# Kernel optimization log

Hardware: AMD Instinct MI355X
Metric: run time of the kernel (lower is better)

The kernel has to match this reference:

```python
import jax, jax.numpy as jnp
import numpy as np
from jax.scipy.special import xlogy

LAMBDA_XM = 0.05
LAMBDA_SEG2D = 1.0
BN_EPS = 1e-5


def setup_inputs() -> dict:
    key = jax.random.key(0)
    ks = jax.random.split(key, 40)
    S, N, Nv, B, Np, M, H, C, MID = 2, 240000, 80000, 2, 120000, 30000, 64, 20, 16
    Nimg = B * M
    f = lambda i, shape, s=0.05: jax.random.normal(ks[i], shape, jnp.float32) * s
    inp = {
        'img_feat': f(0, (S, Nimg, H), 1.0),
        'pts_feat': f(1, (S, Nv, H), 1.0),
        'coors_inv': jax.random.randint(ks[2], (S, N), 0, Nv),
        'labels': jax.random.randint(ks[3], (N,), 0, C),
        'img_label': jax.random.randint(ks[4], (Nimg,), 0, C),
        'p2img_idx': jax.random.randint(ks[5], (B, M), 0, Np),
        # multihead 3d classifiers (per scale): Linear(H,128)-ReLU-Linear(128,C)
        'w3a': f(6, (S, H, 128)), 'b3a': jnp.zeros((S, 128)),
        'w3b': f(7, (S, 128, C)), 'b3b': jnp.zeros((S, C)),
        # multihead fuse classifiers
        'wfa': f(8, (S, H, 128)), 'bfa': jnp.zeros((S, 128)),
        'wfb': f(9, (S, 128, C)), 'bfb': jnp.zeros((S, C)),
        # attention: fc1(H->H//4), fc2(H->H//4), fc3(H//2->2), conv1/conv2 (1x1 -> linear) + BN
        'fc1w': f(10, (S, H, MID)), 'fc1b': jnp.zeros((S, MID)),
        'fc2w': f(11, (S, H, MID)), 'fc2b': jnp.zeros((S, MID)),
        'fc3w': f(12, (S, 2 * MID, 2)), 'fc3b': jnp.zeros((S, 2)),
        'c1w': f(13, (S, H, H)), 'c1b': jnp.zeros((S, H)),
        'bn1g': jnp.ones((S, H)), 'bn1b': jnp.zeros((S, H)),
        'c2w': f(14, (S, H, H)), 'c2b': jnp.zeros((S, H)),
        'bn2g': jnp.ones((S, H)), 'bn2b': jnp.zeros((S, H)),
        # final classifier Linear(S*H,128)-ReLU-Linear(128,C)
        'clw1': f(15, (S * H, 128)), 'clb1': jnp.zeros((128,)),
        'clw2': f(16, (128, C)), 'clb2': jnp.zeros((C,)),
    }
    return inp


def _mlp2(x, w1, b1, w2, b2):
    return jax.nn.relu(x @ w1 + b1) @ w2 + b2


def _ce(logits, lab):
    logp = jax.nn.log_softmax(logits, -1)
    return -jnp.take_along_axis(logp, lab[:, None], axis=1).mean()


def _lovasz(probs, lab):
    # lovasz-softmax over all classes, averaged over present classes
    C = probs.shape[1]
    fg = jax.nn.one_hot(lab, C, dtype=probs.dtype)  # [N,C]
    errors = jnp.abs(fg - probs)

    def per_class(err_c, fg_c):
        order = jnp.argsort(-err_c)
        e = err_c[order]
        f = fg_c[order]
        gts = f.sum()
        inter = gts - jnp.cumsum(f)
        union = gts + jnp.cumsum(1.0 - f)
        jac = 1.0 - inter / union
        jac = jnp.concatenate([jac[:1], jac[1:] - jac[:-1]])
        return jnp.dot(e, jac)

    losses = jax.vmap(per_class)(errors.T, fg.T)  # [C]
    present = (fg.sum(0) > 0).astype(probs.dtype)
    return jnp.sum(losses * present) / jnp.maximum(present.sum(), 1.0)


def _seg_loss(logits, lab):
    return _ce(logits, lab) + _lovasz(jax.nn.softmax(logits, -1), lab)


def _convbn_relu(x, cw, cb, g, b):
    # 1x1 Conv1d == per-point linear; BN (training-mode batch stats over points)
    y = x @ cw + cb
    mu = y.mean(0)
    var = y.var(0)
    return jax.nn.relu((y - mu) * jax.lax.rsqrt(var + BN_EPS) * g + b)


def reference(img_feat, pts_feat, coors_inv, labels, img_label, p2img_idx,
              w3a, b3a, w3b, b3b, wfa, bfa, wfb, bfb,
              fc1w, fc1b, fc2w, fc2b, fc3w, fc3b,
              c1w, c1b, bn1g, bn1b, c2w, c2b, bn2g, bn2b,
              clw1, clb1, clw2, clb2):
    S, Nv, H = pts_feat.shape
    C = w3b.shape[-1]
    B, M = p2img_idx.shape
    N = labels.shape[0]
    Np = N // B
    # p2img_mapping: per-batch gather composed to one global gather (batch blocks are contiguous/equal)
    gidx = (jnp.arange(B)[:, None] * Np + p2img_idx).reshape(-1)  # [Nimg]

    loss = jnp.float32(0.0)
    feats = []
    for s in range(S):
        pred3d = _mlp2(pts_feat[s], w3a[s], b3a[s], w3b[s], b3b[s])  # [Nv,C]
        # voxelize_labels: majority vote per voxel (== unique+scatter_max count argmax)
        counts = jnp.zeros((Nv, C), jnp.float32).at[coors_inv[s], labels].add(1.0)
        vox_lab = jnp.argmax(counts, axis=1)  # [Nv]
        # gather voxel feats/preds to image-projected points (fused gather)
        idx = coors_inv[s][gidx]  # [Nimg]
        p = pts_feat[s][idx]      # [Nimg,H] pseudo feats
        pts_pred = pred3d[idx]    # [Nimg,C]
        v = img_feat[s]           # [Nimg,H] valid (image) feats
        # Attention fusion
        w = jax.nn.sigmoid(
            jnp.concatenate([p @ fc1w[s] + fc1b[s], v @ fc2w[s] + fc2b[s]], -1) @ fc3w[s] + fc3b[s])  # [Nimg,2]
        fuse = (_convbn_relu(p, c1w[s], c1b[s], bn1g[s], bn1b[s]) * w[:, 0:1]
                + _convbn_relu(v, c2w[s], c2b[s], bn2g[s], bn2b[s]) * w[:, 1:2])
        feats.append(fuse)
        fuse_pred = _mlp2(fuse, wfa[s], bfa[s], wfb[s], bfb[s])
        loss = loss + _seg_loss(pred3d, vox_lab)
        loss = loss + _seg_loss(fuse_pred, img_label) * LAMBDA_SEG2D / S
        # F.kl_div(log_softmax(pts_pred), softmax(fuse_pred)), reduction='mean' over all elements
        pf = jax.nn.softmax(fuse_pred, -1)
        kl = jnp.mean(xlogy(pf, pf) - pf * jax.nn.log_softmax(pts_pred, -1))
        loss = loss + kl * LAMBDA_XM / S
    img_logits = _mlp2(jnp.concatenate(feats, -1), clw1, clb1, clw2, clb2)
    loss = loss + _seg_loss(img_logits, img_label)
    return loss
```

## Files before the change

kernel.cpp:

```cpp
#include <hip/hip_runtime.h>
#include <stdint.h>

static constexpr int NV   = 80000;
static constexpr int NPT  = 240000;
static constexpr int NIMG = 60000;
static constexpr int Hh   = 64;
static constexpr int Cc   = 20;
static constexpr int NPp  = 120000;
static constexpr int Mm   = 30000;
static constexpr int NB     = 8192;
static constexpr int NCH    = 16;
static constexpr int NBLK_GA  = (NIMG + 63) / 64;
static constexpr int NBLK_MLP = NV / 64;
static constexpr int NBLK_CNT = (NPT + 255) / 256;
static constexpr int NBLK_FILL_NV = (NV + 255) / 256;
static constexpr int NBLK_FILL_NI = (NIMG + 255) / 256;
static constexpr int NBLK_HIST = Cc * NCH;
static constexpr int NBLK_IDX  = (NIMG + 255) / 256;
#define BN_EPS 1e-5f

using bf16x8 = __attribute__((ext_vector_type(8))) short;
using f32x4  = __attribute__((ext_vector_type(4))) float;

__device__ __forceinline__ float waveReduce(float v) {
  #pragma unroll
  for (int o = 32; o > 0; o >>= 1) v += __shfl_down(v, o);
  return v;
}
__device__ __forceinline__ short f2bf(float f) {
  uint32_t u = __float_as_uint(f);
  return (short)((u + 0x7FFFu + ((u >> 16) & 1u)) >> 16);
}
__device__ __forceinline__ float bf2f(uint32_t h) { return __uint_as_float(h << 16); }
__device__ __forceinline__ uint32_t pk2(float a, float b) {
  return ((uint32_t)(uint16_t)f2bf(a)) | ((uint32_t)(uint16_t)f2bf(b) << 16);
}

struct PackDesc { const float* src; short* dst; int K, Nr, nt; };
struct PackArgs { PackDesc d[14]; };

__global__ void __launch_bounds__(256)
k_pack_zero(PackArgs pa,
            const float* __restrict__ fc1w, const float* __restrict__ fc1b,
            const float* __restrict__ fc2w, const float* __restrict__ fc2b,
            const float* __restrict__ fc3w, const float* __restrict__ fc3b,
            float* __restrict__ attEffs,
            uint4* __restrict__ zb, int zq,
            const int* __restrict__ ci0, const int* __restrict__ ci1,
            const int* __restrict__ p2img,
// ... 28 lines not shown
      int k = kt * 32 + (lane >> 4) * 8 + j;
      int n = nt * 16 + (lane & 15);
      float v = (n < Nr) ? src[(size_t)k * Nr + n] : 0.f;
      dst[idx] = f2bf(v);
    }
  }
  if (bid < 2 && threadIdx.x < 64) {
    int s = bid, t = threadIdx.x;
    const float* f1w = fc1w + s * 64 * 16; const float* f1b = fc1b + s * 16;
    const float* f2w = fc2w + s * 64 * 16; const float* f2b = fc2b + s * 16;
    const float* f3w = fc3w + s * 64;      const float* f3b = fc3b + s * 2;
    float* aE = attEffs + s * 320;
    float p0 = 0.f, p1 = 0.f, v0 = 0.f, v1 = 0.f;
    #pragma unroll
    for (int j = 0; j < 16; j++) {
      p0 = fmaf(f1w[t * 16 + j], f3w[j * 2], p0);
      p1 = fmaf(f1w[t * 16 + j], f3w[j * 2 + 1], p1);
      v0 = fmaf(f2w[t * 16 + j], f3w[(16 + j) * 2], v0);
      v1 = fmaf(f2w[t * 16 + j], f3w[(16 + j) * 2 + 1], v1);
    }
    aE[t * 2] = p0; aE[t * 2 + 1] = p1;
    aE[128 + t * 2] = v0; aE[128 + t * 2 + 1] = v1;
    if (t == 0) {
      float b0 = f3b[0], b1 = f3b[1];
      for (int j = 0; j < 16; j++) {
        b0 += f1b[j] * f3w[j * 2] + f2b[j] * f3w[(16 + j) * 2];
        b1 += f1b[j] * f3w[j * 2 + 1] + f2b[j] * f3w[(16 + j) * 2 + 1];
      }
      aE[256] = b0; aE[257] = b1;
    }
  }
}

__device__ void scanbin_body(const uint32_t* __restrict__ Hb, const uint32_t* __restrict__ HFb,
                             int n, int call, float* __restrict__ lossesC5,
                             int* __restrict__ gts5, int cls) {
  __shared__ int sWC[4], sWF[4];
  __shared__ float sRedF[4];
  int t = threadIdx.x;
  int lane = t & 63, w = t >> 6;
  const uint32_t* Hc  = Hb  + (size_t)cls * NB;
  const uint32_t* HFc = HFb + (size_t)cls * NB;
  int locC = 0, locF = 0;
  #pragma unroll
  for (int i = 0; i < 8; i++) {
    uint4 cv = *(const uint4*)(Hc  + t * 32 + i * 4);
    uint4 fv = *(const uint4*)(HFc + t * 32 + i * 4);
    locC += (int)(cv.x + cv.y + cv.z + cv.w);
    locF += (int)(fv.x + fv.y + fv.z + fv.w);
  }
  int sc = locC, sf = locF;
  #pragma unroll
  for (int o = 1; o < 64; o <<= 1) {
    int a = __shfl_up(sc, o);
    int b = __shfl_up(sf, o);
    if (lane >= o) { sc += a; sf += b; }
  }
  if (lane == 63) { sWC[w] = sc; sWF[w] = sf; }
  __syncthreads();
  int offC = 0, offF = 0, Ftot = 0;
  #pragma unroll
  for (int ww = 0; ww < 4; ww++) {
    int fc = sWF[ww];
    Ftot += fc;
    if (ww < w) { offC += sWC[ww]; offF += fc; }
  }
  int runC = offC + sc - locC;
  int runF = offF + sf - locF;
  float gts = (float)Ftot;
  float contrib = 0.f;
  #pragma unroll
  for (int i = 0; i < 8; i++) {
    uint4 cv = *(const uint4*)(Hc  + t * 32 + i * 4);
    uint4 fv = *(const uint4*)(HFc + t * 32 + i * 4);
    uint32_t ca[4] = {cv.x, cv.y, cv.z, cv.w};
    uint32_t fa[4] = {fv.x, fv.y, fv.z, fv.w};
    #pragma unroll
    for (int j = 0; j < 4; j++) {
      int cnt = (int)ca[j], fgc = (int)fa[j];
      runC += cnt; runF += fgc;
      if (cnt > 0 && Ftot > 0) {
        float r0 = (float)(n - runC);
        float F0 = (float)(Ftot - runF);
        float r1 = r0 + (float)cnt;
        float F1 = F0 + (float)fgc;
        float emean = __uint_as_float((uint32_t)(t * 32 + i * 4 + j) << 17);
        contrib += emean * (r1 / (gts + r1 - F1) - r0 / (gts + r0 - F0));
      }
    }
  }
  contrib = waveReduce(contrib);
  if (lane == 0) sRedF[w] = contrib;
  __syncthreads();
  if (t == 0) {
    lossesC5[call * 32 + cls] = (Ftot > 0) ? (sRedF[0] + sRedF[1] + sRedF[2] + sRedF[3]) : 0.f;
    gts5[call * 32 + cls] = Ftot;
  }
}

template<int D>
__device__ __forceinline__ void mfma_mlp_body(const short* sXb, short* sH,
    int r0, int rows,
    const short* __restrict__ pw1, const float* __restrict__ B1,
    const short* __restrict__ pw2, const float* __restrict__ B2,
    float* __restrict__ Out) {
  constexpr int LDB = D + 8;
  constexpr int KT1 = D / 32;
  const int t = threadIdx.x;
  const int lane = t & 63, w = t >> 6;
  const int m = lane & 15, quad = lane >> 4;
  const int rowA = 16 * w + m;
  bf16x8 a1[KT1];
  #pragma unroll
  for (int kt = 0; kt < KT1; kt++)
    a1[kt] = *(const bf16x8*)(sXb + rowA * LDB + kt * 32 + quad * 8);
  const bf16x8* b1 = (const bf16x8*)pw1;
  #pragma unroll
  for (int nt = 0; nt < 8; nt++) {
    f32x4 c = {0.f, 0.f, 0.f, 0.f};
    #pragma unroll
    for (int kt = 0; kt < KT1; kt++)
      c = __builtin_amdgcn_mfma_f32_16x16x32_bf16(a1[kt], b1[(kt * 8 + nt) * 64 + lane], c, 0, 0, 0);
    int col = nt * 16 + m;
    float bc = B1[col];
    #pragma unroll
    for (int reg = 0; reg < 4; reg++)
      sH[(16 * w + quad * 4 + reg) * 136 + col] = f2bf(fmaxf(c[reg] + bc, 0.f));
  }
  __syncthreads();
  bf16x8 a2[4];
  #pragma unroll
  for (int kt = 0; kt < 4; kt++)
    a2[kt] = *(const bf16x8*)(sH + rowA * 136 + kt * 32 + quad * 8);
  const bf16x8* b2 = (const bf16x8*)pw2;
  #pragma unroll
  for (int nt = 0; nt < 2; nt++) {
    f32x4 c = {0.f, 0.f, 0.f, 0.f};
    #pragma unroll
    for (int kt = 0; kt < 4; kt++)
      c = __builtin_amdgcn_mfma_f32_16x16x32_bf16(a2[kt], b2[(kt * 2 + nt) * 64 + lane], c, 0, 0, 0);
    int col = nt * 16 + m;
    if (col < Cc) {
      float bc = B2[col];
      #pragma unroll
      for (int reg = 0; reg < 4; reg++) {
        int gr = r0 + 16 * w + quad * 4 + reg;
        if (gr < rows) Out[(size_t)gr * Cc + col] = c[reg] + bc;
      }
    }
  }
}

__device__ void mlp64_body(int bid0, const float* __restrict__ X,
    const short* __restrict__ pw1, const float* __restrict__ B1,
    const short* __restrict__ pw2, const float* __restrict__ B2,
    float* __restrict__ Out, int rows, char* smem) {
  short* sXb = (short*)smem;
  short* sH  = (short*)(smem + 9216);
  int t = threadIdx.x, r0 = bid0 * 64;
  for (int i = t; i < 1024; i += 256) {
    int r = i >> 4, k4 = (i & 15) * 4;
    int gr = r0 + r;
    float4 v = (gr < rows) ? *(const float4*)(X + (size_t)gr * 64 + k4)
                           : make_float4(0.f, 0.f, 0.f, 0.f);
    uint2 p; p.x = pk2(v.x, v.y); p.y = pk2(v.z, v.w);
    *(uint2*)(sXb + r * 72 + k4) = p;
  }
  __syncthreads();
  mfma_mlp_body<64>(sXb, sH, r0, rows, pw1, B1, pw2, B2, Out);
}

__device__ void mlp128_body(int bid0, const uint16_t* __restrict__ Xh,
    const short* __restrict__ pw1, const float* __restrict__ B1,
    const short* __restrict__ pw2, const float* __restrict__ B2,
    float* __restrict__ Out, char* smem) {
  short* sXb = (short*)smem;
  short* sH  = (short*)(smem + 17408);
  int t = threadIdx.x, r0 = bid0 * 64;
  for (int i = t; i < 2048; i += 256) {
    int r = i >> 5, k4 = (i & 31) * 4;
    int gr = r0 + r;
    uint2 p = (gr < NIMG) ? *(const uint2*)(Xh + (size_t)gr * 128 + k4) : make_uint2(0u, 0u);
    *(uint2*)(sXb + r * 136 + k4) = p;
  }
  __syncthreads();
  mfma_mlp_body<128>(sXb, sH, r0, NIMG, pw1, B1, pw2, B2, Out);
}

__device__ void cnt_body(int bid0, const int* __restrict__ ci, const int* __restrict__ labels,
                         int* __restrict__ counts) {
  int i = bid0 * 256 + threadIdx.x;
  if (i < NPT) atomicAdd(&counts[(size_t)ci[i] * Cc + labels[i]], 1);
}

__device__ void colred_body(int bid0, const float* __restrict__ partials,
                            float* __restrict__ red64) {
  int t = threadIdx.x, j = bid0;
  float v = 0.f;
  for (int b = j; b < NBLK_GA; b += 64) v += partials[(size_t)b * 256 + t];
  red64[j * 256 + t] = v;
}

__device__ void fill_body(int bid0, const float* __restrict__ logits,
                          const int* __restrict__ lab, const int* __restrict__ vcnt,
                          int n, uint16_t* __restrict__ E,
                          float ceScale, float* __restrict__ lossAcc,
                          const float* __restrict__ pred3d, const int* __restrict__ idxg,
                          float klScale) {
  int i = bid0 * 256 + threadIdx.x;
  float total = 0.f;
  if (i < n) {
    int lb;
    if (vcnt) {
      const int* crow = vcnt + (size_t)i * Cc;
      int best = crow[0], arg = 0;
      #pragma unroll
      for (int k = 1; k < Cc; k++) {
        int ck = crow[k];
        if (ck > best) { best = ck; arg = k; }
      }
      lb = arg;
    } else {
      lb = lab[i];
    }
    const float* l = logits + (size_t)i * Cc;
    float m = l[0];
    #pragma unroll
    for (int c = 1; c < Cc; c++) m = fmaxf(m, l[c]);
    float ex[Cc]; float se = 0.f;
    #pragma unroll
    for (int c = 0; c < Cc; c++) { ex[c] = expf(l[c] - m); se += ex[c]; }
    float inv = 1.f / se;
    float lse = logf(se);
    total = -(l[lb] - m - lse) * ceScale;
    #pragma unroll
    for (int c = 0; c < Cc; c++) {
      float prob = ex[c] * inv;
      int fg = (c == lb) ? 1 : 0;
      float err = fg ? (1.f - prob) : prob;
      err = fmaxf(err, 0.f);
      uint32_t key = __float_as_uint(err) >> 17;
      E[(size_t)c * n + i] = (uint16_t)((key << 1) | (uint32_t)fg);
    }
    if (pred3d) {
      const float* q = pred3d + (size_t)idxg[i] * Cc;
      float mq = q[0];
      #pragma unroll
      for (int c = 1; c < Cc; c++) mq = fmaxf(mq, q[c]);
      float sq = 0.f;
      #pragma unroll
      for (int c = 0; c < Cc; c++) sq += expf(q[c] - mq);
      float lsq = logf(sq);
      float kl = 0.f;
      #pragma unroll
      for (int c = 0; c < Cc; c++) {
        float lf = l[c] - m - lse;
        float pf = ex[c] * inv;
        float lq = q[c] - mq - lsq;
        kl += pf * (lf - lq);
      }
      total += kl * klScale;
    }
  }
  total = waveReduce(total);
  __shared__ float sh[4];
  int lane = threadIdx.x & 63, w = threadIdx.x >> 6;
  if (lane == 0) sh[w] = total;
  __syncthreads();
  if (threadIdx.x == 0) atomicAdd(lossAcc, sh[0] + sh[1] + sh[2] + sh[3]);
}

__device__ void hist_body(int bid0, const uint16_t* __restrict__ E, int n,
                          uint32_t* __restrict__ H, uint32_t* __restrict__ HF, char* smem) {
  uint32_t* lcf = (uint32_t*)smem;
  int t = threadIdx.x;
  int cls = bid0 / NCH, ch = bid0 - cls * NCH;
  int CHsz = (n + NCH - 1) / NCH;
  int i0 = ch * CHsz;
  int i1 = min(n, i0 + CHsz);
  for (int b = t; b < NB; b += 256) lcf[b] = 0u;
  __syncthreads();
  const uint16_t* Ec = E + (size_t)cls * n;
  for (int i = i0 + t; i < i1; i += 256) {
    uint32_t p = Ec[i];
    atomicAdd(&lcf[p >> 1], 0x10000u | (p & 1u));
  }
  __syncthreads();
  uint32_t* Hc  = H  + (size_t)cls * NB;
  uint32_t* HFc = HF + (size_t)cls * NB;
  for (int b = t; b < NB; b += 256) {
    uint32_t v = lcf[b];
    if (v) {
      atomicAdd(&Hc[b], v >> 16);
      uint32_t f = v & 0xFFFFu;
      if (f) atomicAdd(&HFc[b], f);
    }
  }
}

__device__ void gatt_body(int bid0, const float* __restrict__ pts, const int* __restrict__ idx,
                          const float* __restrict__ img,
                          const short* __restrict__ pc1, const float* __restrict__ c1b,
                          const short* __restrict__ pc2, const float* __restrict__ c2b,
                          const float* __restrict__ attEff,
                          uint16_t* __restrict__ y1, uint16_t* __restrict__ y2,
                          float* __restrict__ attw, float* __restrict__ partials,
                          char* smem) {
  short* sP = (short*)smem;
  short* sV = (short*)(smem + 9216);
  float* sAtt  = (float*)(smem + 18432);
  float* sStat = (float*)(smem + 20480);
  int t = threadIdx.x;
  int r0 = bid0 * 64;
  for (int i = t; i < 1024; i += 256) {
    int r = i >> 4, q = i & 15;
    int gr = r0 + r;
    float4 vp = make_float4(0.f, 0.f, 0.f, 0.f), vv = vp;
    if (gr < NIMG) {
      vp = *(const float4*)(pts + (size_t)idx[gr] * 64 + q * 4);
      vv = *(const float4*)(img + (size_t)gr * 64 + q * 4);
    }
    uint2 pp, qv;
    pp.x = pk2(vp.x, vp.y); pp.y = pk2(vp.z, vp.w);
    qv.x = pk2(vv.x, vv.y); qv.y = pk2(vv.z, vv.w);
    *(uint2*)(sP + r * 72 + q * 4) = pp;
    *(uint2*)(sV + r * 72 + q * 4) = qv;
  }
  __syncthreads();
  {
// ... 64 lines not shown
      base[32] = s2;
      base[48] = q2;
    }
  }
  __syncthreads();
  {
    int kind = t >> 6, col = t & 63;
    int nt = col >> 4, mm = col & 15;
    float v = 0.f;
    #pragma unroll
    for (int ww = 0; ww < 4; ww++)
      v += sStat[(ww * 4 + nt) * 64 + kind * 16 + mm];
    partials[(size_t)bid0 * 256 + kind * 64 + col] = v;
  }
  if (t < 64) {
    int gr = r0 + t;
    if (gr < NIMG) {
      float l0 = attEff[256] + sAtt[t * 8] + sAtt[t * 8 + 2] + sAtt[t * 8 + 4] + sAtt[t * 8 + 6];
      float l1 = attEff[257] + sAtt[t * 8 + 1] + sAtt[t * 8 + 3] + sAtt[t * 8 + 5] + sAtt[t * 8 + 7];
      attw[gr * 2]     = 1.f / (1.f + expf(-l0));
      attw[gr * 2 + 1] = 1.f / (1.f + expf(-l1));
    }
  }
}

__device__ void fusemlp_body(int bid0,
    const uint16_t* __restrict__ y1, const uint16_t* __restrict__ y2,
    const float* __restrict__ attw, const float* __restrict__ red64,
    const float* __restrict__ g1, const float* __restrict__ be1,
    const float* __restrict__ g2, const float* __restrict__ be2,
    uint16_t* __restrict__ feats, int s64,
    const short* __restrict__ pw1, const float* __restrict__ B1,
    const short* __restrict__ pw2, const float* __restrict__ B2,
    float* __restrict__ Out, char* smem) {
  short* sXb = (short*)smem;
  short* sH  = (short*)(smem + 9216);
  float* sBn = (float*)(smem + 9216 + 17408);
  int t = threadIdx.x, r0 = bid0 * 64;
  float acc = 0.f;
  #pragma unroll 8
  for (int b = 0; b < 64; b++) acc += red64[b * 256 + t];
  float* sSum = (float*)sH;
  sSum[t] = acc;
  __syncthreads();
  if (t < 64) {
    float nn = (float)NIMG;
    float mu1 = sSum[t] / nn;
    float var1 = sSum[64 + t] / nn - mu1 * mu1;
    float a1 = g1[t] / sqrtf(var1 + BN_EPS);
    sBn[t] = a1; sBn[64 + t] = be1[t] - mu1 * a1;
    float mu2 = sSum[128 + t] / nn;
    float var2 = sSum[192 + t] / nn - mu2 * mu2;
    float a2 = g2[t] / sqrtf(var2 + BN_EPS);
    sBn[128 + t] = a2; sBn[192 + t] = be2[t] - mu2 * a2;
  }
  __syncthreads();
  for (int i = t; i < 1024; i += 256) {
    int r = i >> 4, q = i & 15;
    int gr = r0 + r;
    uint2 zp = make_uint2(0u, 0u);
    if (gr < NIMG) {
      float4 a1 = *(const float4*)(sBn + q * 4);
      float4 c1 = *(const float4*)(sBn + 64 + q * 4);
      float4 a2 = *(const float4*)(sBn + 128 + q * 4);
      float4 c2 = *(const float4*)(sBn + 192 + q * 4);
      uint2 u1 = *(const uint2*)(y1 + (size_t)gr * 64 + q * 4);
      uint2 u2 = *(const uint2*)(y2 + (size_t)gr * 64 + q * 4);
      float w0 = attw[gr * 2], w1 = attw[gr * 2 + 1];
      float zx = fmaxf(fmaf(bf2f(u1.x & 0xffff), a1.x, c1.x), 0.f) * w0
               + fmaxf(fmaf(bf2f(u2.x & 0xffff), a2.x, c2.x), 0.f) * w1;
      float zy = fmaxf(fmaf(bf2f(u1.x >> 16),   a1.y, c1.y), 0.f) * w0
               + fmaxf(fmaf(bf2f(u2.x >> 16),   a2.y, c2.y), 0.f) * w1;
      float zz = fmaxf(fmaf(bf2f(u1.y & 0xffff), a1.z, c1.z), 0.f) * w0
               + fmaxf(fmaf(bf2f(u2.y & 0xffff), a2.z, c2.z), 0.f) * w1;
      float zw = fmaxf(fmaf(bf2f(u1.y >> 16),   a1.w, c1.w), 0.f) * w0
               + fmaxf(fmaf(bf2f(u2.y >> 16),   a2.w, c2.w), 0.f) * w1;
      zp.x = pk2(zx, zy); zp.y = pk2(zz, zw);
      *(uint2*)(feats + (size_t)gr * 128 + s64 + q * 4) = zp;
    }
    *(uint2*)(sXb + r * 72 + q * 4) = zp;
  }
  __syncthreads();
  mfma_mlp_body<64>(sXb, sH, r0, NIMG, pw1, B1, pw2, B2, Out);
}

__global__ void __launch_bounds__(256)
k_mega2(const float* __restrict__ pf0, const float* __restrict__ pf1,
        const int* __restrict__ idx0, const int* __restrict__ idx1,
        const float* __restrict__ if0, const float* __restrict__ if1,
        const short* pc1w0, const short* pc1w1, const short* pc2w0, const short* pc2w1,
        const float* c1b, const float* c2b, const float* attEffs,
        uint16_t* y1a, uint16_t* y2a, uint16_t* y1b, uint16_t* y2b,
        float* attw0, float* attw1, float* partials0, float* partials1,
        const short* pw3a0, const float* b3a, const short* pw3b0, const float* b3b,
        const short* pw3a1, const short* pw3b1,
        float* pred3d0, float* pred3d1,
        const int* __restrict__ ci0, const int* __restrict__ ci1,
        const int* __restrict__ labels,
        int* __restrict__ counts0, int* __restrict__ counts1) {
  __shared__ char smem[26624];
  int bid = blockIdx.x;
  if (bid < NBLK_GA) {
    gatt_body(bid, pf0, idx0, if0, pc1w0, c1b, pc2w0, c2b, attEffs,
              y1a, y2a, attw0, partials0, smem);
    return;
  }
  bid -= NBLK_GA;
  if (bid < NBLK_GA) {
    gatt_body(bid, pf1, idx1, if1, pc1w1, c1b + 64, pc2w1, c2b + 64, attEffs + 320,
              y1b, y2b, attw1, partials1, smem);
    return;
  }
  bid -= NBLK_GA;
  if (bid < NBLK_MLP) { mlp64_body(bid, pf0, pw3a0, b3a, pw3b0, b3b, pred3d0, NV, smem); return; }
  bid -= NBLK_MLP;
  if (bid < NBLK_MLP) { mlp64_body(bid, pf1, pw3a1, b3a + 128, pw3b1, b3b + Cc, pred3d1, NV, smem); return; }
  bid -= NBLK_MLP;
  if (bid < NBLK_CNT) { cnt_body(bid, ci0, labels, counts0); return; }
  cnt_body(bid - NBLK_CNT, ci1, labels, counts1);
}

__global__ void __launch_bounds__(256)
k_fill_colred(const float* __restrict__ l0, const int* __restrict__ vc0, uint16_t* __restrict__ E0,
              const float* __restrict__ l1, const int* __restrict__ vc1, uint16_t* __restrict__ E1,
              float ce, float* __restrict__ lossAcc,
              const float* partials0, float* red64_0,
              const float* partials1, float* red64_1) {
  int bid = blockIdx.x;
  if (bid < NBLK_FILL_NV) {
    fill_body(bid, l0, nullptr, vc0, NV, E0, ce, lossAcc, nullptr, nullptr, 0.f);
    return;
  }
  bid -= NBLK_FILL_NV;
  if (bid < NBLK_FILL_NV) {
    fill_body(bid, l1, nullptr, vc1, NV, E1, ce, lossAcc, nullptr, nullptr, 0.f);
    return;
  }
  bid -= NBLK_FILL_NV;
  if (bid < 64) { colred_body(bid, partials0, red64_0); return; }
  colred_body(bid - 64, partials1, red64_1);
}

__global__ void __launch_bounds__(256)
k_fuse2_hist2(const uint16_t* y1a, const uint16_t* y2a, const float* attw0, const float* red64_0,
              const uint16_t* y1b, const uint16_t* y2b, const float* attw1, const float* red64_1,
              const float* bn1g, const float* bn1b, const float* bn2g, const float* bn2b,
              uint16_t* feats,
              const short* pwfa0, const float* bfa, const short* pwfb0, const float* bfb,
              const short* pwfa1, const short* pwfb1,
              float* fusepred0, float* fusepred1,
              const uint16_t* __restrict__ E0, uint32_t* H0, uint32_t* HF0,
              const uint16_t* __restrict__ E1, uint32_t* H2, uint32_t* HF2) {
  __shared__ char smem[32768];
  int bid = blockIdx.x;
  if (bid < NBLK_GA) {
    fusemlp_body(bid, y1a, y2a, attw0, red64_0, bn1g, bn1b, bn2g, bn2b, feats, 0,
                 pwfa0, bfa, pwfb0, bfb, fusepred0, smem);
    return;
  }
  bid -= NBLK_GA;
  if (bid < NBLK_GA) {
    fusemlp_body(bid, y1b, y2b, attw1, red64_1, bn1g + 64, bn1b + 64, bn2g + 64, bn2b + 64,
                 feats, 64, pwfa1, bfa + 128, pwfb1, bfb + Cc, fusepred1, smem);
    return;
  }
  bid -= NBLK_GA;
  if (bid < NBLK_HIST) { hist_body(bid, E0, NV, H0, HF0, smem); return; }
  hist_body(bid - NBLK_HIST, E1, NV, H2, HF2, smem);
}

__global__ void __launch_bounds__(256)
k_finx2(const uint16_t* __restrict__ feats,
        const short* pcl1, const float* clb1, const short* pcl2, const float* clb2,
        float* finalpred,
        const float* fusepred0, const float* pred3d0, const int* idx0, uint16_t* E0w,
        const float* fusepred1, const float* pred3d1, const int* idx1, uint16_t* E1w,
        const int* __restrict__ img_label, float ce, float kl, float* lossAcc,
        const uint32_t* H0, const uint32_t* HF0,
        const uint32_t* H2, const uint32_t* HF2,
        float* lossesC5, int* gts5) {
  __shared__ char smem[34816];
  int bid = blockIdx.x;
  if (bid < NBLK_GA) { mlp128_body(bid, feats, pcl1, clb1, pcl2, clb2, finalpred, smem); return; }
  bid -= NBLK_GA;
  if (bid < NBLK_FILL_NI) {
    fill_body(bid, fusepred0, img_label, nullptr, NIMG, E0w, ce, lossAcc, pred3d0, idx0, kl);
    return;
  }
  bid -= NBLK_FILL_NI;
  if (bid < NBLK_FILL_NI) {
    fill_body(bid, fusepred1, img_label, nullptr, NIMG, E1w, ce, lossAcc, pred3d1, idx1, kl);
    return;
  }
  bid -= NBLK_FILL_NI;
  if (bid < Cc) { scanbin_body(H0, HF0, NV, 0, lossesC5, gts5, bid); return; }
  scanbin_body(H2, HF2, NV, 2, lossesC5, gts5, bid - Cc);
}

__global__ void __launch_bounds__(256)
k_hist2_fill(const uint16_t* __restrict__ E0, uint32_t* H1, uint32_t* HF1,
             const uint16_t* __restrict__ E1, uint32_t* H3, uint32_t* HF3,
             const float* __restrict__ finalpred, const int* __restrict__ img_label,
             uint16_t* __restrict__ E2, float ce, float* lossAcc) {
  __shared__ char smem[32768];
  int bid = blockIdx.x;
  if (bid < NBLK_HIST) { hist_body(bid, E0, NIMG, H1, HF1, smem); return; }
  bid -= NBLK_HIST;
  if (bid < NBLK_HIST) { hist_body(bid, E1, NIMG, H3, HF3, smem); return; }
  fill_body(bid - NBLK_HIST, finalpred, img_label, nullptr, NIMG, E2, ce, lossAcc,
            nullptr, nullptr, 0.f);
}

__global__ void __launch_bounds__(256)
k_hist_scan2(const uint16_t* __restrict__ E2, uint32_t* H4, uint32_t* HF4,
             const uint32_t* H1, const uint32_t* HF1,
             const uint32_t* H3, const uint32_t* HF3,
             float* lossesC5, int* gts5) {
  __shared__ char smem[32768];
  int bid = blockIdx.x;
  if (bid < NBLK_HIST) { hist_body(bid, E2, NIMG, H4, HF4, smem); return; }
  bid -= NBLK_HIST;
  if (bid < Cc) { scanbin_body(H1, HF1, NIMG, 1, lossesC5, gts5, bid); return; }
  scanbin_body(H3, HF3, NIMG, 3, lossesC5, gts5, bid - Cc);
}

__global__ void __launch_bounds__(256)
k_scanbin5(const uint32_t* Hb, const uint32_t* HFb, int n, int call,
           float* lossesC5, int* gts5) {
  scanbin_body(Hb, HFb, n, call, lossesC5, gts5, blockIdx.x);
}

__global__ void k_final(const float* __restrict__ lossAcc,
                        const float* __restrict__ lossesC5, const int* __restrict__ gts5,
                        float* __restrict__ out) {
  const float coefs[5] = {1.0f, 0.5f, 1.0f, 0.5f, 1.0f};
  float loss = lossAcc[0];
  for (int call = 0; call < 5; call++) {
    float s = 0.f; int np = 0;
    for (int c = 0; c < Cc; c++)
      if (gts5[call * 32 + c] > 0) { s += lossesC5[call * 32 + c]; np++; }
    loss += coefs[call] * s / (float)(np > 0 ? np : 1);
  }
  out[0] = loss;
}

extern "C" void kernel_launch(void* const* d_in, const int* in_sizes, int n_in,
                              void* d_out, int out_size, void* d_ws, size_t ws_size,
                              hipStream_t stream) {
  const float* img_feat = (const float*)d_in[0];
  const float* pts_feat = (const float*)d_in[1];
  const int* coors_inv  = (const int*)d_in[2];
  const int* labels     = (const int*)d_in[3];
  const int* img_label  = (const int*)d_in[4];
  const int* p2img      = (const int*)d_in[5];
  const float* w3a = (const float*)d_in[6];
  const float* b3a = (const float*)d_in[7];
  const float* w3b = (const float*)d_in[8];
  const float* b3b = (const float*)d_in[9];
  const float* wfa = (const float*)d_in[10];
  const float* bfa = (const float*)d_in[11];
  const float* wfb = (const float*)d_in[12];
  const float* bfb = (const float*)d_in[13];
// ... 2 lines not shown
  const float* fc2w = (const float*)d_in[16];
  const float* fc2b = (const float*)d_in[17];
  const float* fc3w = (const float*)d_in[18];
  const float* fc3b = (const float*)d_in[19];
  const float* c1w  = (const float*)d_in[20];
  const float* c1b  = (const float*)d_in[21];
  const float* bn1g = (const float*)d_in[22];
  const float* bn1b = (const float*)d_in[23];
  const float* c2w  = (const float*)d_in[24];
  const float* c2b  = (const float*)d_in[25];
  const float* bn2g = (const float*)d_in[26];
  const float* bn2b = (const float*)d_in[27];
  const float* clw1 = (const float*)d_in[28];
  const float* clb1 = (const float*)d_in[29];
  const float* clw2 = (const float*)d_in[30];
  const float* clb2 = (const float*)d_in[31];
  (void)in_sizes; (void)n_in; (void)out_size; (void)ws_size;

  char* ws = (char*)d_ws;
  size_t off = 0;
  auto alloc = [&](size_t bytes) { void* p = ws + off; off += (bytes + 255) & ~(size_t)255; return p; };
  uint16_t* feats = (uint16_t*)alloc((size_t)NIMG * 128 * 2);
  float* pred3d0 = (float*)alloc((size_t)NV * Cc * 4);
  float* pred3d1 = (float*)alloc((size_t)NV * Cc * 4);
  int* idx0 = (int*)alloc((size_t)NIMG * 4);
  int* idx1 = (int*)alloc((size_t)NIMG * 4);
  uint16_t* y1a = (uint16_t*)alloc((size_t)NIMG * Hh * 2);
  uint16_t* y2a = (uint16_t*)alloc((size_t)NIMG * Hh * 2);
  uint16_t* y1b = (uint16_t*)alloc((size_t)NIMG * Hh * 2);
  uint16_t* y2b = (uint16_t*)alloc((size_t)NIMG * Hh * 2);
  uint16_t* E0 = (uint16_t*)alloc((size_t)Cc * NV * 2);
  uint16_t* E1 = (uint16_t*)alloc((size_t)Cc * NV * 2);
  uint16_t* E2 = (uint16_t*)alloc((size_t)Cc * NIMG * 2);
  float* partials0 = (float*)alloc((size_t)NBLK_GA * 256 * 4);
  float* partials1 = (float*)alloc((size_t)NBLK_GA * 256 * 4);
  float* red64_0 = (float*)alloc(64 * 256 * 4);
  float* red64_1 = (float*)alloc(64 * 256 * 4);
  float* attw0 = (float*)alloc((size_t)NIMG * 2 * 4);
  float* attw1 = (float*)alloc((size_t)NIMG * 2 * 4);
  float* fusepred0 = (float*)alloc((size_t)NIMG * Cc * 4);
  float* fusepred1 = (float*)alloc((size_t)NIMG * Cc * 4);
  float* finalpred = (float*)alloc((size_t)NIMG * Cc * 4);
  short* pwAll = (short*)alloc(86016 * 2);
  short* pw3a0 = pwAll,          * pw3a1 = pwAll + 8192;
  short* pwfa0 = pwAll + 16384,  * pwfa1 = pwAll + 24576;
  short* pw3b0 = pwAll + 32768,  * pw3b1 = pwAll + 36864;
  short* pwfb0 = pwAll + 40960,  * pwfb1 = pwAll + 45056;
  short* pcl1  = pwAll + 49152;
  short* pcl2  = pwAll + 65536;
  short* pc1w0 = pwAll + 69632,  * pc1w1 = pwAll + 73728;
  short* pc2w0 = pwAll + 77824,  * pc2w1 = pwAll + 81920;
  float* attEffs = (float*)alloc(2 * 320 * 4);
  size_t zsize = 1024 + (size_t)5 * 2 * Cc * NB * 4 + (size_t)2 * NV * Cc * 4;
  char* zbase = (char*)alloc(zsize);
  float* lossAcc  = (float*)zbase;
  float* lossesC5 = (float*)zbase + 32;
  int*   gts5     = (int*)((float*)zbase + 192);
  uint32_t* Hbase = (uint32_t*)(zbase + 1024);
  auto Hc  = [&](int call) { return Hbase + (size_t)call * 2 * Cc * NB; };
  auto HFc = [&](int call) { return Hbase + (size_t)call * 2 * Cc * NB + (size_t)Cc * NB; };
  int* counts0 = (int*)(zbase + 1024 + (size_t)5 * 2 * Cc * NB * 4);
  int* counts1 = counts0 + (size_t)NV * Cc;
  int zq = (int)(zsize / 16);

  const float kl = 0.025f / ((float)NIMG * Cc);
  const float* pf0 = pts_feat;
  const float* pf1 = pts_feat + (size_t)NV * Hh;
  const float* if0 = img_feat;
  const float* if1 = img_feat + (size_t)NIMG * Hh;
  const int* ci0 = coors_inv;
  const int* ci1 = coors_inv + NPT;

  PackArgs pa;
  pa.d[0]  = {w3a,        pw3a0, 64, 128, 8};
  pa.d[1]  = {w3a + 8192, pw3a1, 64, 128, 8};
  pa.d[2]  = {wfa,        pwfa0, 64, 128, 8};
  pa.d[3]  = {wfa + 8192, pwfa1, 64, 128, 8};
  pa.d[4]  = {w3b,        pw3b0, 128, 20, 2};
  pa.d[5]  = {w3b + 2560, pw3b1, 128, 20, 2};
  pa.d[6]  = {wfb,        pwfb0, 128, 20, 2};
  pa.d[7]  = {wfb + 2560, pwfb1, 128, 20, 2};
  pa.d[8]  = {clw1,       pcl1, 128, 128, 8};
  pa.d[9]  = {clw2,       pcl2, 128, 20, 2};
  pa.d[10] = {c1w,        pc1w0, 64, 64, 4};
  pa.d[11] = {c1w + 4096, pc1w1, 64, 64, 4};
  pa.d[12] = {c2w,        pc2w0, 64, 64, 4};
  pa.d[13] = {c2w + 4096, pc2w1, 64, 64, 4};
  k_pack_zero<<<384 + 2 * NBLK_IDX, 256, 0, stream>>>(
      pa, fc1w, fc1b, fc2w, fc2b, fc3w, fc3b, attEffs,
      (uint4*)zbase, zq, ci0, ci1, p2img, idx0, idx1);

  k_mega2<<<2 * NBLK_GA + 2 * NBLK_MLP + 2 * NBLK_CNT, 256, 0, stream>>>(
      pf0, pf1, idx0, idx1, if0, if1,
      pc1w0, pc1w1, pc2w0, pc2w1, c1b, c2b, attEffs,
      y1a, y2a, y1b, y2b, attw0, attw1, partials0, partials1,
      pw3a0, b3a, pw3b0, b3b, pw3a1, pw3b1, pred3d0, pred3d1,
      ci0, ci1, labels, counts0, counts1);

  k_fill_colred<<<2 * NBLK_FILL_NV + 128, 256, 0, stream>>>(
      pred3d0, counts0, E0, pred3d1, counts1, E1, 1.0f / NV, lossAcc,
      partials0, red64_0, partials1, red64_1);

  k_fuse2_hist2<<<2 * NBLK_GA + 2 * NBLK_HIST, 256, 0, stream>>>(
      y1a, y2a, attw0, red64_0, y1b, y2b, attw1, red64_1,
      bn1g, bn1b, bn2g, bn2b, feats,
      pwfa0, bfa, pwfb0, bfb, pwfa1, pwfb1, fusepred0, fusepred1,
      E0, Hc(0), HFc(0), E1, Hc(2), HFc(2));

  k_finx2<<<NBLK_GA + 2 * NBLK_FILL_NI + 2 * Cc, 256, 0, stream>>>(
      feats, pcl1, clb1, pcl2, clb2, finalpred,
      fusepred0, pred3d0, idx0, E0,
      fusepred1, pred3d1, idx1, E1,
      img_label, 0.5f / NIMG, kl, lossAcc,
      Hc(0), HFc(0), Hc(2), HFc(2), lossesC5, gts5);

  k_hist2_fill<<<2 * NBLK_HIST + NBLK_FILL_NI, 256, 0, stream>>>(
      E0, Hc(1), HFc(1), E1, Hc(3), HFc(3),
      finalpred, img_label, E2, 1.0f / NIMG, lossAcc);

  k_hist_scan2<<<NBLK_HIST + 2 * Cc, 256, 0, stream>>>(
      E2, Hc(4), HFc(4), Hc(1), HFc(1), Hc(3), HFc(3), lossesC5, gts5);

  k_scanbin5<<<Cc, 256, 0, stream>>>(Hc(4), HFc(4), NIMG, 4, lossesC5, gts5);

  k_final<<<1, 1, 0, stream>>>(lossAcc, lossesC5, gts5, (float*)d_out);
}
```

Measured before the change: 347.1 us.

## Fuse loss/error computation into MLP epilogues and pack histogram bins into 64-bit

The fuse-MLP and final-classifier kernels now keep their logits in LDS and compute CE, KL and Lovasz error keys directly in a tile epilogue. This removes the fusepred/finalpred global buffers and the separate fill passes, which drops one kernel launch and reshuffles the histogram work into earlier kernels. Count and foreground histograms are merged into one interleaved 64-bit array, so each bin takes a single 64-bit atomic and scans do one vector load per pair. The cost is that only 64 of 256 threads per block run the epilogue loss, and separate E3/E4 buffers are added.

```diff
diff --git a/kernel.cpp b/kernel.cpp
--- a/kernel.cpp
+++ b/kernel.cpp
@@ -14,7 +14,6 @@
 static constexpr int NBLK_MLP = NV / 64;
 static constexpr int NBLK_CNT = (NPT + 255) / 256;
 static constexpr int NBLK_FILL_NV = (NV + 255) / 256;
-static constexpr int NBLK_FILL_NI = (NIMG + 255) / 256;
 static constexpr int NBLK_HIST = Cc * NCH;
 static constexpr int NBLK_IDX  = (NIMG + 255) / 256;
 #define BN_EPS 1e-5f
@@ -109,22 +108,20 @@
   }
 }
 
-__device__ void scanbin_body(const uint32_t* __restrict__ Hb, const uint32_t* __restrict__ HFb,
+__device__ void scanbin_body(const unsigned long long* __restrict__ H64,
                              int n, int call, float* __restrict__ lossesC5,
                              int* __restrict__ gts5, int cls) {
   __shared__ int sWC[4], sWF[4];
   __shared__ float sRedF[4];
   int t = threadIdx.x;
   int lane = t & 63, w = t >> 6;
-  const uint32_t* Hc  = Hb  + (size_t)cls * NB;
-  const uint32_t* HFc = HFb + (size_t)cls * NB;
+  const uint4* Hv = (const uint4*)(H64 + (size_t)cls * NB + (size_t)t * 32);
   int locC = 0, locF = 0;
   #pragma unroll
-  for (int i = 0; i < 8; i++) {
-    uint4 cv = *(const uint4*)(Hc  + t * 32 + i * 4);
-    uint4 fv = *(const uint4*)(HFc + t * 32 + i * 4);
-    locC += (int)(cv.x + cv.y + cv.z + cv.w);
-    locF += (int)(fv.x + fv.y + fv.z + fv.w);
+  for (int i = 0; i < 16; i++) {
+    uint4 u = Hv[i];
+    locF += (int)(u.x + u.z);
+    locC += (int)(u.y + u.w);
   }
   int sc = locC, sf = locF;
   #pragma unroll
@@ -147,21 +144,18 @@
   float gts = (float)Ftot;
   float contrib = 0.f;
   #pragma unroll
-  for (int i = 0; i < 8; i++) {
-    uint4 cv = *(const uint4*)(Hc  + t * 32 + i * 4);
-    uint4 fv = *(const uint4*)(HFc + t * 32 + i * 4);
-    uint32_t ca[4] = {cv.x, cv.y, cv.z, cv.w};
-    uint32_t fa[4] = {fv.x, fv.y, fv.z, fv.w};
-    #pragma unroll
-    for (int j = 0; j < 4; j++) {
-      int cnt = (int)ca[j], fgc = (int)fa[j];
+  for (int i = 0; i < 16; i++) {
+    uint4 u = Hv[i];
+    #pragma unroll
+    for (int j = 0; j < 2; j++) {
+      int cnt = (int)(j ? u.w : u.y), fgc = (int)(j ? u.z : u.x);
       runC += cnt; runF += fgc;
       if (cnt > 0 && Ftot > 0) {
         float r0 = (float)(n - runC);
         float F0 = (float)(Ftot - runF);
         float r1 = r0 + (float)cnt;
         float F1 = F0 + (float)fgc;
-        float emean = __uint_as_float((uint32_t)(t * 32 + i * 4 + j) << 17);
+        float emean = __uint_as_float((uint32_t)(t * 32 + i * 2 + j) << 17);
         contrib += emean * (r1 / (gts + r1 - F1) - r0 / (gts + r0 - F0));
       }
     }
@@ -175,8 +169,63 @@
   }
 }
 
-template<int D>
-__device__ __forceinline__ void mfma_mlp_body(const short* sXb, short* sH,
+__device__ void tile_loss(const float* __restrict__ sL, int r0, int rows, int n,
+                          const int* __restrict__ lab, uint16_t* __restrict__ E,
+                          float ceScale, float* __restrict__ lossAcc,
+                          const float* __restrict__ pred3d, const int* __restrict__ idxg,
+                          float klScale) {
+  int t = threadIdx.x;
+  if (t < 64) {
+    float total = 0.f;
+    int gr = r0 + t;
+    if (gr < rows) {
+      const float* l = sL + t * 21;
+      float m = l[0];
+      #pragma unroll
+      for (int c = 1; c < Cc; c++) m = fmaxf(m, l[c]);
+      float ex[Cc]; float se = 0.f;
+      #pragma unroll
+      for (int c = 0; c < Cc; c++) { ex[c] = expf(l[c] - m); se += ex[c]; }
+      float inv = 1.f / se;
+      float lse = logf(se);
+      int lb = lab[gr];
+      total = -(l[lb] - m - lse) * ceScale;
+      #pragma unroll
+      for (int c = 0; c < Cc; c++) {
+        float prob = ex[c] * inv;
+        int fg = (c == lb) ? 1 : 0;
+        float err = fg ? (1.f - prob) : prob;
+        err = fmaxf(err, 0.f);
+        uint32_t key = __float_as_uint(err) >> 17;
+        E[(size_t)c * n + gr] = (uint16_t)((key << 1) | (uint32_t)fg);
+      }
+      if (pred3d) {
+        const float* q = pred3d + (size_t)idxg[gr] * Cc;
+        float mq = q[0];
+        #pragma unroll
+        for (int c = 1; c < Cc; c++) mq = fmaxf(mq, q[c]);
+        float sq = 0.f;
+        #pragma unroll
+        for (int c = 0; c < Cc; c++) sq += expf(q[c] - mq);
+        float lsq = logf(sq);
+        float kl = 0.f;
+        #pragma unroll
+        for (int c = 0; c < Cc; c++) {
+          float lf = l[c] - m - lse;
+          float pf = ex[c] * inv;
+          float lq = q[c] - mq - lsq;
+          kl += pf * (lf - lq);
+        }
+        total += kl * klScale;
+      }
+    }
+    total = waveReduce(total);
+    if (t == 0) atomicAdd(lossAcc, total);
+  }
+}
+
+template<int D, bool TO_LDS>
+__device__ __forceinline__ void mfma_mlp_core(const short* sXb, short* sH, float* sL,
     int r0, int rows,
     const short* __restrict__ pw1, const float* __restrict__ B1,
     const short* __restrict__ pw2, const float* __restrict__ B2,
@@ -221,8 +270,13 @@
       float bc = B2[col];
       #pragma unroll
       for (int reg = 0; reg < 4; reg++) {
-        int gr = r0 + 16 * w + quad * 4 + reg;
-        if (gr < rows) Out[(size_t)gr * Cc + col] = c[reg] + bc;
+        int rr = 16 * w + quad * 4 + reg;
+        if (TO_LDS) {
+          sL[rr * 21 + col] = c[reg] + bc;
+        } else {
+          int gr = r0 + rr;
+          if (gr < rows) Out[(size_t)gr * Cc + col] = c[reg] + bc;
+        }
       }
     }
   }
@@ -244,13 +298,14 @@
     *(uint2*)(sXb + r * 72 + k4) = p;
   }
   __syncthreads();
-  mfma_mlp_body<64>(sXb, sH, r0, rows, pw1, B1, pw2, B2, Out);
-}
-
-__device__ void mlp128_body(int bid0, const uint16_t* __restrict__ Xh,
+  mfma_mlp_core<64, false>(sXb, sH, nullptr, r0, rows, pw1, B1, pw2, B2, Out);
+}
+
+__device__ void mlp128_loss_body(int bid0, const uint16_t* __restrict__ Xh,
     const short* __restrict__ pw1, const float* __restrict__ B1,
     const short* __restrict__ pw2, const float* __restrict__ B2,
-    float* __restrict__ Out, char* smem) {
+    const int* __restrict__ lab, uint16_t* __restrict__ E, float ce,
+    float* __restrict__ lossAcc, char* smem) {
   short* sXb = (short*)smem;
   short* sH  = (short*)(smem + 17408);
   int t = threadIdx.x, r0 = bid0 * 64;
@@ -261,7 +316,9 @@
     *(uint2*)(sXb + r * 136 + k4) = p;
   }
   __syncthreads();
-  mfma_mlp_body<128>(sXb, sH, r0, NIMG, pw1, B1, pw2, B2, Out);
+  mfma_mlp_core<128, true>(sXb, sH, (float*)sXb, r0, NIMG, pw1, B1, pw2, B2, nullptr);
+  __syncthreads();
+  tile_loss((float*)sXb, r0, NIMG, NIMG, lab, E, ce, lossAcc, nullptr, nullptr, 0.f);
 }
 
 __device__ void cnt_body(int bid0, const int* __restrict__ ci, const int* __restrict__ labels,
@@ -279,26 +336,18 @@
 }
 
 __device__ void fill_body(int bid0, const float* __restrict__ logits,
-                          const int* __restrict__ lab, const int* __restrict__ vcnt,
+                          const int* __restrict__ vcnt,
                           int n, uint16_t* __restrict__ E,
-                          float ceScale, float* __restrict__ lossAcc,
-                          const float* __restrict__ pred3d, const int* __restrict__ idxg,
-                          float klScale) {
+                          float ceScale, float* __restrict__ lossAcc) {
   int i = bid0 * 256 + threadIdx.x;
   float total = 0.f;
   if (i < n) {
-    int lb;
-    if (vcnt) {
-      const int* crow = vcnt + (size_t)i * Cc;
-      int best = crow[0], arg = 0;
-      #pragma unroll
-      for (int k = 1; k < Cc; k++) {
-        int ck = crow[k];
-        if (ck > best) { best = ck; arg = k; }
-      }
-      lb = arg;
-    } else {
-      lb = lab[i];
+    const int* crow = vcnt + (size_t)i * Cc;
+    int best = crow[0], lb = 0;
+    #pragma unroll
+    for (int k = 1; k < Cc; k++) {
+      int ck = crow[k];
+      if (ck > best) { best = ck; lb = k; }
     }
     const float* l = logits + (size_t)i * Cc;
     float m = l[0];
@@ -319,25 +368,6 @@
       uint32_t key = __float_as_uint(err) >> 17;
       E[(size_t)c * n + i] = (uint16_t)((key << 1) | (uint32_t)fg);
     }
-    if (pred3d) {
-      const float* q = pred3d + (size_t)idxg[i] * Cc;
-      float mq = q[0];
-      #pragma unroll
-      for (int c = 1; c < Cc; c++) mq = fmaxf(mq, q[c]);
-      float sq = 0.f;
-      #pragma unroll
-      for (int c = 0; c < Cc; c++) sq += expf(q[c] - mq);
-      float lsq = logf(sq);
-      float kl = 0.f;
-      #pragma unroll
-      for (int c = 0; c < Cc; c++) {
-        float lf = l[c] - m - lse;
-        float pf = ex[c] * inv;
-        float lq = q[c] - mq - lsq;
-        kl += pf * (lf - lq);
-      }
-      total += kl * klScale;
-    }
   }
   total = waveReduce(total);
   __shared__ float sh[4];
@@ -348,7 +378,7 @@
 }
 
 __device__ void hist_body(int bid0, const uint16_t* __restrict__ E, int n,
-                          uint32_t* __restrict__ H, uint32_t* __restrict__ HF, char* smem) {
+                          unsigned long long* __restrict__ H64, char* smem) {
   uint32_t* lcf = (uint32_t*)smem;
   int t = threadIdx.x;
   int cls = bid0 / NCH, ch = bid0 - cls * NCH;
@@ -363,15 +393,11 @@
     atomicAdd(&lcf[p >> 1], 0x10000u | (p & 1u));
   }
   __syncthreads();
-  uint32_t* Hc  = H  + (size_t)cls * NB;
-  uint32_t* HFc = HF + (size_t)cls * NB;
+  unsigned long long* Hc = H64 + (size_t)cls * NB;
   for (int b = t; b < NB; b += 256) {
     uint32_t v = lcf[b];
-    if (v) {
-      atomicAdd(&Hc[b], v >> 16);
-      uint32_t f = v & 0xFFFFu;
-      if (f) atomicAdd(&HFc[b], f);
-    }
+    if (v)
+      atomicAdd(&Hc[b], ((unsigned long long)(v >> 16) << 32) | (v & 0xFFFFu));
   }
 }
 
@@ -502,7 +528,9 @@
     uint16_t* __restrict__ feats, int s64,
     const short* __restrict__ pw1, const float* __restrict__ B1,
     const short* __restrict__ pw2, const float* __restrict__ B2,
-    float* __restrict__ Out, char* smem) {
+    const int* __restrict__ lab, uint16_t* __restrict__ E, float ce,
+    const float* __restrict__ pred3d, const int* __restrict__ idxg, float klScale,
+    float* __restrict__ lossAcc, char* smem) {
   short* sXb = (short*)smem;
   short* sH  = (short*)(smem + 9216);
   float* sBn = (float*)(smem + 9216 + 17408);
@@ -551,7 +579,9 @@
     *(uint2*)(sXb + r * 72 + q * 4) = zp;
   }
   __syncthreads();
-  mfma_mlp_body<64>(sXb, sH, r0, NIMG, pw1, B1, pw2, B2, Out);
+  mfma_mlp_core<64, true>(sXb, sH, (float*)sXb, r0, NIMG, pw1, B1, pw2, B2, nullptr);
+  __syncthreads();
+  tile_loss((float*)sXb, r0, NIMG, NIMG, lab, E, ce, lossAcc, pred3d, idxg, klScale);
 }
 
 __global__ void __launch_bounds__(256)
@@ -598,12 +628,12 @@
               const float* partials1, float* red64_1) {
   int bid = blockIdx.x;
   if (bid < NBLK_FILL_NV) {
-    fill_body(bid, l0, nullptr, vc0, NV, E0, ce, lossAcc, nullptr, nullptr, 0.f);
+    fill_body(bid, l0, vc0, NV, E0, ce, lossAcc);
     return;
   }
   bid -= NBLK_FILL_NV;
   if (bid < NBLK_FILL_NV) {
-    fill_body(bid, l1, nullptr, vc1, NV, E1, ce, lossAcc, nullptr, nullptr, 0.f);
+    fill_body(bid, l1, vc1, NV, E1, ce, lossAcc);
     return;
   }
   bid -= NBLK_FILL_NV;
@@ -618,86 +648,70 @@
               uint16_t* feats,
               const short* pwfa0, const float* bfa, const short* pwfb0, const float* bfb,
               const short* pwfa1, const short* pwfb1,
-              float* fusepred0, float* fusepred1,
-              const uint16_t* __restrict__ E0, uint32_t* H0, uint32_t* HF0,
-              const uint16_t* __restrict__ E1, uint32_t* H2, uint32_t* HF2) {
+              const int* __restrict__ img_label, float ce, float kl, float* lossAcc,
+              const float* pred3d0, const int* idx0, uint16_t* E3,
+              const float* pred3d1, const int* idx1, uint16_t* E4,
+              const uint16_t* __restrict__ E0, unsigned long long* H0,
+              const uint16_t* __restrict__ E1, unsigned long long* H2) {
   __shared__ char smem[32768];
   int bid = blockIdx.x;
   if (bid < NBLK_GA) {
     fusemlp_body(bid, y1a, y2a, attw0, red64_0, bn1g, bn1b, bn2g, bn2b, feats, 0,
-                 pwfa0, bfa, pwfb0, bfb, fusepred0, smem);
+                 pwfa0, bfa, pwfb0, bfb,
+                 img_label, E3, ce, pred3d0, idx0, kl, lossAcc, smem);
     return;
   }
   bid -= NBLK_GA;
   if (bid < NBLK_GA) {
     fusemlp_body(bid, y1b, y2b, attw1, red64_1, bn1g + 64, bn1b + 64, bn2g + 64, bn2b + 64,
-                 feats, 64, pwfa1, bfa + 128, pwfb1, bfb + Cc, fusepred1, smem);
+                 feats, 64, pwfa1, bfa + 128, pwfb1, bfb + Cc,
+                 img_label, E4, ce, pred3d1, idx1, kl, lossAcc, smem);
     return;
   }
   bid -= NBLK_GA;
-  if (bid < NBLK_HIST) { hist_body(bid, E0, NV, H0, HF0, smem); return; }
-  hist_body(bid - NBLK_HIST, E1, NV, H2, HF2, smem);
+  if (bid < NBLK_HIST) { hist_body(bid, E0, NV, H0, smem); return; }
+  hist_body(bid - NBLK_HIST, E1, NV, H2, smem);
 }
 
 __global__ void __launch_bounds__(256)
 k_finx2(const uint16_t* __restrict__ feats,
         const short* pcl1, const float* clb1, const short* pcl2, const float* clb2,
-        float* finalpred,
-        const float* fusepred0, const float* pred3d0, const int* idx0, uint16_t* E0w,
-        const float* fusepred1, const float* pred3d1, const int* idx1, uint16_t* E1w,
-        const int* __restrict__ img_label, float ce, float kl, float* lossAcc,
-        const uint32_t* H0, const uint32_t* HF0,
-        const uint32_t* H2, const uint32_t* HF2,
+        const int* __restrict__ img_label, uint16_t* E2, float ce, float* lossAcc,
+        const uint16_t* __restrict__ E3, unsigned long long* H1,
+        const uint16_t* __restrict__ E4, unsigned long long* H3,
+        const unsigned long long* H0, const unsigned long long* H2,
         float* lossesC5, int* gts5) {
   __shared__ char smem[34816];
   int bid = blockIdx.x;
-  if (bid < NBLK_GA) { mlp128_body(bid, feats, pcl1, clb1, pcl2, clb2, finalpred, smem); return; }
+  if (bid < NBLK_GA) {
+    mlp128_loss_body(bid, feats, pcl1, clb1, pcl2, clb2, img_label, E2, ce, lossAcc, smem);
+    return;
+  }
   bid -= NBLK_GA;
-  if (bid < NBLK_FILL_NI) {
-    fill_body(bid, fusepred0, img_label, nullptr, NIMG, E0w, ce, lossAcc, pred3d0, idx0, kl);
-    return;
-  }
-  bid -= NBLK_FILL_NI;
-  if (bid < NBLK_FILL_NI) {
-    fill_body(bid, fusepred1, img_label, nullptr, NIMG, E1w, ce, lossAcc, pred3d1, idx1, kl);
-    return;
-  }
-  bid -= NBLK_FILL_NI;
-  if (bid < Cc) { scanbin_body(H0, HF0, NV, 0, lossesC5, gts5, bid); return; }
-  scanbin_body(H2, HF2, NV, 2, lossesC5, gts5, bid - Cc);
+  if (bid < NBLK_HIST) { hist_body(bid, E3, NIMG, H1, smem); return; }
+  bid -= NBLK_HIST;
+  if (bid < NBLK_HIST) { hist_body(bid, E4, NIMG, H3, smem); return; }
+  bid -= NBLK_HIST;
+  if (bid < Cc) { scanbin_body(H0, NV, 0, lossesC5, gts5, bid); return; }
+  scanbin_body(H2, NV, 2, lossesC5, gts5, bid - Cc);
 }
 
 __global__ void __launch_bounds__(256)
-k_hist2_fill(const uint16_t* __restrict__ E0, uint32_t* H1, uint32_t* HF1,
-             const uint16_t* __restrict__ E1, uint32_t* H3, uint32_t* HF3,
-             const float* __restrict__ finalpred, const int* __restrict__ img_label,
-             uint16_t* __restrict__ E2, float ce, float* lossAcc) {
-  __shared__ char smem[32768];
-  int bid = blockIdx.x;
-  if (bid < NBLK_HIST) { hist_body(bid, E0, NIMG, H1, HF1, smem); return; }
-  bid -= NBLK_HIST;
-  if (bid < NBLK_HIST) { hist_body(bid, E1, NIMG, H3, HF3, smem); return; }
-  fill_body(bid - NBLK_HIST, finalpred, img_label, nullptr, NIMG, E2, ce, lossAcc,
-            nullptr, nullptr, 0.f);
-}
-
-__global__ void __launch_bounds__(256)
-k_hist_scan2(const uint16_t* __restrict__ E2, uint32_t* H4, uint32_t* HF4,
-             const uint32_t* H1, const uint32_t* HF1,
-             const uint32_t* H3, const uint32_t* HF3,
+k_hist_scan2(const uint16_t* __restrict__ E2, unsigned long long* H4,
+             const unsigned long long* H1, const unsigned long long* H3,
              float* lossesC5, int* gts5) {
   __shared__ char smem[32768];
   int bid = blockIdx.x;
-  if (bid < NBLK_HIST) { hist_body(bid, E2, NIMG, H4, HF4, smem); return; }
+  if (bid < NBLK_HIST) { hist_body(bid, E2, NIMG, H4, smem); return; }
   bid -= NBLK_HIST;
-  if (bid < Cc) { scanbin_body(H1, HF1, NIMG, 1, lossesC5, gts5, bid); return; }
-  scanbin_body(H3, HF3, NIMG, 3, lossesC5, gts5, bid - Cc);
+  if (bid < Cc) { scanbin_body(H1, NIMG, 1, lossesC5, gts5, bid); return; }
+  scanbin_body(H3, NIMG, 3, lossesC5, gts5, bid - Cc);
 }
 
 __global__ void __launch_bounds__(256)
-k_scanbin5(const uint32_t* Hb, const uint32_t* HFb, int n, int call,
+k_scanbin5(const unsigned long long* H64, int n, int call,
            float* lossesC5, int* gts5) {
-  scanbin_body(Hb, HFb, n, call, lossesC5, gts5, blockIdx.x);
+  scanbin_body(H64, n, call, lossesC5, gts5, blockIdx.x);
 }
 
 __global__ void k_final(const float* __restrict__ lossAcc,
@@ -766,15 +780,14 @@
   uint16_t* E0 = (uint16_t*)alloc((size_t)Cc * NV * 2);
   uint16_t* E1 = (uint16_t*)alloc((size_t)Cc * NV * 2);
   uint16_t* E2 = (uint16_t*)alloc((size_t)Cc * NIMG * 2);
+  uint16_t* E3 = (uint16_t*)alloc((size_t)Cc * NIMG * 2);
+  uint16_t* E4 = (uint16_t*)alloc((size_t)Cc * NIMG * 2);
   float* partials0 = (float*)alloc((size_t)NBLK_GA * 256 * 4);
   float* partials1 = (float*)alloc((size_t)NBLK_GA * 256 * 4);
   float* red64_0 = (float*)alloc(64 * 256 * 4);
   float* red64_1 = (float*)alloc(64 * 256 * 4);
   float* attw0 = (float*)alloc((size_t)NIMG * 2 * 4);
   float* attw1 = (float*)alloc((size_t)NIMG * 2 * 4);
-  float* fusepred0 = (float*)alloc((size_t)NIMG * Cc * 4);
-  float* fusepred1 = (float*)alloc((size_t)NIMG * Cc * 4);
-  float* finalpred = (float*)alloc((size_t)NIMG * Cc * 4);
   short* pwAll = (short*)alloc(86016 * 2);
   short* pw3a0 = pwAll,          * pw3a1 = pwAll + 8192;
   short* pwfa0 = pwAll + 16384,  * pwfa1 = pwAll + 24576;
@@ -785,15 +798,14 @@
   short* pc1w0 = pwAll + 69632,  * pc1w1 = pwAll + 73728;
   short* pc2w0 = pwAll + 77824,  * pc2w1 = pwAll + 81920;
   float* attEffs = (float*)alloc(2 * 320 * 4);
-  size_t zsize = 1024 + (size_t)5 * 2 * Cc * NB * 4 + (size_t)2 * NV * Cc * 4;
+  size_t zsize = 1024 + (size_t)5 * Cc * NB * 8 + (size_t)2 * NV * Cc * 4;
   char* zbase = (char*)alloc(zsize);
   float* lossAcc  = (float*)zbase;
   float* lossesC5 = (float*)zbase + 32;
   int*   gts5     = (int*)((float*)zbase + 192);
-  uint32_t* Hbase = (uint32_t*)(zbase + 1024);
-  auto Hc  = [&](int call) { return Hbase + (size_t)call * 2 * Cc * NB; };
-  auto HFc = [&](int call) { return Hbase + (size_t)call * 2 * Cc * NB + (size_t)Cc * NB; };
-  int* counts0 = (int*)(zbase + 1024 + (size_t)5 * 2 * Cc * NB * 4);
+  unsigned long long* Hbase = (unsigned long long*)(zbase + 1024);
+  auto Hc = [&](int call) { return Hbase + (size_t)call * Cc * NB; };
+  int* counts0 = (int*)(zbase + 1024 + (size_t)5 * Cc * NB * 8);
   int* counts1 = counts0 + (size_t)NV * Cc;
   int zq = (int)(zsize / 16);
 
@@ -838,24 +850,21 @@
   k_fuse2_hist2<<<2 * NBLK_GA + 2 * NBLK_HIST, 256, 0, stream>>>(
       y1a, y2a, attw0, red64_0, y1b, y2b, attw1, red64_1,
       bn1g, bn1b, bn2g, bn2b, feats,
-      pwfa0, bfa, pwfb0, bfb, pwfa1, pwfb1, fusepred0, fusepred1,
-      E0, Hc(0), HFc(0), E1, Hc(2), HFc(2));
-
-  k_finx2<<<NBLK_GA + 2 * NBLK_FILL_NI + 2 * Cc, 256, 0, stream>>>(
-      feats, pcl1, clb1, pcl2, clb2, finalpred,
-      fusepred0, pred3d0, idx0, E0,
-      fusepred1, pred3d1, idx1, E1,
+      pwfa0, bfa, pwfb0, bfb, pwfa1, pwfb1,
       img_label, 0.5f / NIMG, kl, lossAcc,
-      Hc(0), HFc(0), Hc(2), HFc(2), lossesC5, gts5);
-
-  k_hist2_fill<<<2 * NBLK_HIST + NBLK_FILL_NI, 256, 0, stream>>>(
-      E0, Hc(1), HFc(1), E1, Hc(3), HFc(3),
-      finalpred, img_label, E2, 1.0f / NIMG, lossAcc);
+      pred3d0, idx0, E3, pred3d1, idx1, E4,
+      E0, Hc(0), E1, Hc(2));
+
+  k_finx2<<<NBLK_GA + 2 * NBLK_HIST + 2 * Cc, 256, 0, stream>>>(
+      feats, pcl1, clb1, pcl2, clb2,
+      img_label, E2, 1.0f / NIMG, lossAcc,
+      E3, Hc(1), E4, Hc(3),
+      Hc(0), Hc(2), lossesC5, gts5);
 
   k_hist_scan2<<<NBLK_HIST + 2 * Cc, 256, 0, stream>>>(
-      E2, Hc(4), HFc(4), Hc(1), HFc(1), Hc(3), HFc(3), lossesC5, gts5);
-
-  k_scanbin5<<<Cc, 256, 0, stream>>>(Hc(4), HFc(4), NIMG, 4, lossesC5, gts5);
+      E2, Hc(4), Hc(1), Hc(3), lossesC5, gts5);
+
+  k_scanbin5<<<Cc, 256, 0, stream>>>(Hc(4), NIMG, 4, lossesC5, gts5);
 
   k_final<<<1, 1, 0, stream>>>(lossAcc, lossesC5, gts5, (float*)d_out);
 }
```

After: 355.9 us. 2.5% more time.
